# Kernel optimization log

Measured on AMD Instinct MI355X. Metric: run time of the kernel, lower is better.

The kernel has to match this reference:

```python
import jax, jax.numpy as jnp
import numpy as np

H = 512          # hidden_dim
S = 64           # num_symbols
MAXLEN = 128     # maxlen['target']
SOS = 0          # symb2int['<sos>']


def _gru_cell(x, h, Wih, Whh, bih, bhh):
    # PyTorch GRU cell. x: (N, in), h: (N, H)
    gi = x @ Wih.T + bih          # (N, 3H)
    gh = h @ Whh.T + bhh          # (N, 3H)
    ir, iz, inn = jnp.split(gi, 3, axis=-1)
    hr, hz, hn = jnp.split(gh, 3, axis=-1)
    r = jax.nn.sigmoid(ir + hr)
    z = jax.nn.sigmoid(iz + hz)
    n = jnp.tanh(inn + r * hn)
    return (1.0 - z) * n + z * h


def setup_inputs() -> dict:
    key = jax.random.key(0)
    ks = jax.random.split(key, 16)
    N, Lsrc = 128, 512
    s = 1.0 / np.sqrt(H)
    inp = {
        "x": jax.random.normal(ks[0], (N, 2, Lsrc), dtype=jnp.float32),
        "target": jax.random.randint(ks[1], (N, MAXLEN), 0, S),
        # encoder GRU (input size 2)
        "enc_Wih": jax.random.normal(ks[2], (3 * H, 2), dtype=jnp.float32) * s,
        "enc_Whh": jax.random.normal(ks[3], (3 * H, H), dtype=jnp.float32) * s,
        "enc_bih": jax.random.normal(ks[4], (3 * H,), dtype=jnp.float32) * s,
        "enc_bhh": jax.random.normal(ks[5], (3 * H,), dtype=jnp.float32) * s,
        # decoder GRU (input size H)
        "dec_Wih": jax.random.normal(ks[6], (3 * H, H), dtype=jnp.float32) * s,
        "dec_Whh": jax.random.normal(ks[7], (3 * H, H), dtype=jnp.float32) * s,
        "dec_bih": jax.random.normal(ks[8], (3 * H,), dtype=jnp.float32) * s,
        "dec_bhh": jax.random.normal(ks[9], (3 * H,), dtype=jnp.float32) * s,
        # decoder embedding, attention FF, output head
        "emb": jax.random.normal(ks[10], (S, H), dtype=jnp.float32),
        "attn_ff_W": jax.random.normal(ks[11], (H, 2 * H), dtype=jnp.float32) * s,
        "attn_ff_b": jnp.zeros((H,), dtype=jnp.float32),
        "fc_W": jax.random.normal(ks[12], (S, H), dtype=jnp.float32) * s,
        "fc_b": jnp.zeros((S,), dtype=jnp.float32),
    }
    return inp


def reference(x, target, enc_Wih, enc_Whh, enc_bih, enc_bhh,
              dec_Wih, dec_Whh, dec_bih, dec_bhh,
              emb, attn_ff_W, attn_ff_b, fc_W, fc_b):
    N = x.shape[0]
    # ---- encoder: x (N, 2, L) -> (L, N, 2), scan GRU over time ----
    xs = jnp.transpose(x, (2, 0, 1))                      # (L, N, 2)
    h0 = jnp.zeros((N, H), dtype=x.dtype)

    def enc_step(h, xt):
        h2 = _gru_cell(xt, h, enc_Wih, enc_Whh, enc_bih, enc_bhh)
        return h2, h2

    enc_hN, enc_ys = jax.lax.scan(enc_step, h0, xs)
    enc_out = jnp.transpose(enc_ys, (1, 0, 2))            # (N, L, H)

    # ---- decoder with attention, fully teacher-forced (target given) ----
    # tokens fed at step i: sos for i=0, target[:, i-1] afterwards
    toks = jnp.concatenate(
        [jnp.full((N, 1), SOS, dtype=target.dtype), target[:, :MAXLEN - 1]], axis=1)
    emb_seq = emb[toks]                                   # (N, MAXLEN, H)
    emb_seq = jnp.transpose(emb_seq, (1, 0, 2))           # (MAXLEN, N, H)

    def dec_step(h, e):
        q = _gru_cell(e, h, dec_Wih, dec_Whh, dec_bih, dec_bhh)   # (N, H)
        scores = jnp.einsum('nh,nlh->nl', q, enc_out)             # (N, L)
        w = jax.nn.softmax(scores, axis=-1)
        attn = jnp.einsum('nl,nlh->nh', w, enc_out)               # (N, H)
        ff = jnp.concatenate([q, attn], axis=-1) @ attn_ff_W.T + attn_ff_b
        dec = ff @ fc_W.T + fc_b                                  # (N, S)
        return q, (dec, w)

    dec_hN, (v_out, all_w) = jax.lax.scan(dec_step, enc_hN, emb_seq)
    v_out = jnp.transpose(v_out, (1, 0, 2))               # (N, MAXLEN, S)
    all_w = jnp.transpose(all_w, (1, 0, 2))               # (N, MAXLEN, L)
    return v_out, dec_hN[None, :, :], all_w
```

## Files before the change

### kernel.cpp

```cpp
#include <hip/hip_runtime.h>
#include <math.h>

#define H   512
#define S   64
#define T   128
#define NB  128
#define L   512

#define OFF_ENC   0u
#define OFF_Q     33554432u
#define OFF_ATTN  41943040u
#define OFF_DGI   50331648u
#define OFF_M4    50429952u
#define OFF_C     50495488u
#define OFF_FLG1  50495552u
#define OFF_FLG2  50503744u

#define OUT_V  0
#define OUT_HN 1048576
#define OUT_W  1114112

__device__ __forceinline__ float sigmoidf_(float x){ return 1.0f/(1.0f+expf(-x)); }

#define FLAG_ST(p, v) __hip_atomic_store((p), (v), __ATOMIC_RELAXED, __HIP_MEMORY_SCOPE_AGENT)
#define FLAG_LD(p)    __hip_atomic_load((p), __ATOMIC_RELAXED, __HIP_MEMORY_SCOPE_AGENT)
#define ATOM_STF(p, v) __hip_atomic_store((p), (v), __ATOMIC_RELAXED, __HIP_MEMORY_SCOPE_AGENT)
#define ATOM_LD8(p)    __hip_atomic_load((const unsigned long long*)(p), __ATOMIC_RELAXED, __HIP_MEMORY_SCOPE_AGENT)

#define GLOAD4(dst, addr) \
  asm volatile("global_load_dwordx4 %0, %1, off" : "=v"(dst) : "v"(addr))

__global__ void prep_m_kernel(float* __restrict__ M4, float* __restrict__ c,
                              const float* __restrict__ aW, const float* __restrict__ aB,
                              const float* __restrict__ fcW, const float* __restrict__ fcB){
  int idx = blockIdx.x*256 + threadIdx.x;
  int k = idx >> 6, s = idx & 63;
  float acc = 0.f;
  for (int o = 0; o < H; ++o) acc += aW[(size_t)o*1024 + k] * fcW[(size_t)s*H + o];
  int k4 = k >> 2, kk = k & 3;
  M4[(size_t)(k4*64 + s)*4 + kk] = acc;
  if (idx < 64){
    float a2 = 0.f;
    for (int o = 0; o < H; ++o) a2 += aB[o] * fcW[(size_t)idx*H + o];
    c[idx] = a2 + fcB[idx];
  }
}

__global__ __launch_bounds__(256) void dgi_kernel(
    float* __restrict__ dgi, const float* __restrict__ Wih,
    const float* __restrict__ bih, const float* __restrict__ emb){
  __shared__ __align__(16) float wsm[4][H];
  int b = blockIdx.x;
  int tid = threadIdx.x;
  int jl = tid >> 6, s = tid & 63;
  for (int jj = 0; jj < 6; ++jj){
    int j0 = b*24 + jj*4;
    __syncthreads();
    for (int e = tid; e < 512; e += 256){
      int r = e >> 7, kv = e & 127;
      ((float4*)&wsm[r][0])[kv] = *(const float4*)&Wih[(size_t)(j0+r)*H + kv*4];
    }
    __syncthreads();
    int j = j0 + jl;
    float acc = bih[j];
    #pragma unroll 4
    for (int k4 = 0; k4 < 128; ++k4){
      float4 w4 = ((const float4*)&wsm[jl][0])[k4];
      float4 e4 = *(const float4*)&emb[(size_t)s*H + k4*4];
      acc = fmaf(w4.x,e4.x, fmaf(w4.y,e4.y, fmaf(w4.z,e4.z, fmaf(w4.w,e4.w, acc))));
    }
    dgi[(size_t)s*1536 + j] = acc;
  }
}

__global__ __attribute__((amdgpu_flat_work_group_size(512,512), amdgpu_waves_per_eu(2,2)))
void enc_persist(
    float* __restrict__ enc, const float* __restrict__ x,
    const float* __restrict__ Wih, const float* __restrict__ Whh,
    const float* __restrict__ bih, const float* __restrict__ bhh,
    int* __restrict__ flags){
  __shared__ __align__(16) float hs[4*H];
  const int tid = threadIdx.x;
  const int jh_l = tid >> 3;
  const int kg   = tid & 7;
  const int g  = blockIdx.x & 31;
  const int jb = blockIdx.x >> 5;
  const int jh = jb*64 + jh_l;
  const int n0 = g*4;
  int* fl = flags + g*8*32;

  float4 wr[16], wz[16], wn[16];
  #pragma unroll
  for (int i = 0; i < 16; ++i){
    const float* p0 = &Whh[(size_t)jh*H        + (kg + 8*i)*4];
    const float* p1 = &Whh[(size_t)(512+jh)*H  + (kg + 8*i)*4];
    const float* p2 = &Whh[(size_t)(1024+jh)*H + (kg + 8*i)*4];
    GLOAD4(wr[i], p0);
    GLOAD4(wz[i], p1);
    GLOAD4(wn[i], p2);
  }
  asm volatile("s_waitcnt vmcnt(0)" ::: "memory");

  const float wir0 = Wih[jh*2],        wir1 = Wih[jh*2+1];
  const float wiz0 = Wih[(512+jh)*2],  wiz1 = Wih[(512+jh)*2+1];
  const float win0 = Wih[(1024+jh)*2], win1 = Wih[(1024+jh)*2+1];
  const float br  = bih[jh] + bhh[jh];
  const float bz  = bih[512+jh] + bhh[512+jh];
  const float bin = bih[1024+jh], bhn = bhh[1024+jh];
  const int nr = kg & 3;
  const int n = n0 + nr;
  const int sr = tid >> 7;
  const int sv = tid & 127;

  for (int t = 0; t < L; ++t){
    float x0 = x[(size_t)n*1024 + t], x1 = x[(size_t)n*1024 + 512 + t];
    if (t == 0){
      ((float4*)hs)[tid] = make_float4(0,0,0,0);
      __syncthreads();
    } else {
      if (tid < 8){
        while (FLAG_LD(&fl[tid*32]) < t) __builtin_amdgcn_s_sleep(1);
      }
      __syncthreads();
      const float* srcp = &enc[((size_t)(n0+sr)*L + (t-1))*H + sv*4];
      unsigned long long a = ATOM_LD8(srcp);
      unsigned long long b = ATOM_LD8(srcp+2);
      unsigned long long* dst = (unsigned long long*)hs;
      dst[(sr*128+sv)*2]   = a;
      dst[(sr*128+sv)*2+1] = b;
      __syncthreads();
    }

    float mar = 0.f, maz = 0.f, man = 0.f;
    #pragma unroll
    for (int nl = 0; nl < 4; ++nl){
      const float4* hb = (const float4*)&hs[nl*H];
      float pr = 0.f, pz = 0.f, pn = 0.f;
      #pragma unroll
      for (int i = 0; i < 16; ++i){
        float4 h4 = hb[kg + 8*i];
        pr = fmaf(h4.x,wr[i].x, fmaf(h4.y,wr[i].y, fmaf(h4.z,wr[i].z, fmaf(h4.w,wr[i].w, pr))));
        pz = fmaf(h4.x,wz[i].x, fmaf(h4.y,wz[i].y, fmaf(h4.z,wz[i].z, fmaf(h4.w,wz[i].w, pz))));
        pn = fmaf(h4.x,wn[i].x, fmaf(h4.y,wn[i].y, fmaf(h4.z,wn[i].z, fmaf(h4.w,wn[i].w, pn))));
      }
      #pragma unroll
      for (int off = 1; off < 8; off <<= 1){
        pr += __shfl_xor(pr, off);
        pz += __shfl_xor(pz, off);
        pn += __shfl_xor(pn, off);
      }
      if (kg == nl){ mar = pr; maz = pz; man = pn; }
    }
    if (kg < 4){
      float rg = sigmoidf_(fmaf(x0,wir0, fmaf(x1,wir1, br))  + mar);
      float zg = sigmoidf_(fmaf(x0,wiz0, fmaf(x1,wiz1, bz))  + maz);
      float ng = tanhf    (fmaf(x0,win0, fmaf(x1,win1, bin)) + rg*(man + bhn));
      float hp = hs[nr*H + jh];
      ATOM_STF(&enc[((size_t)n*L + t)*H + jh], (1.f - zg)*ng + zg*hp);
    }
    asm volatile("s_waitcnt vmcnt(0)" ::: "memory");
    __syncthreads();
    if (tid == 0) FLAG_ST(&fl[jb*32], t+1);
  }
}

__global__ __attribute__((amdgpu_flat_work_group_size(512,512), amdgpu_waves_per_eu(2,2)))
void dec_persist(
    const float* __restrict__ enc, float* __restrict__ q_all,
    const int* __restrict__ tgt, const float* __restrict__ dgi,
    const float* __restrict__ Whh, const float* __restrict__ bhh,
    float* __restrict__ hn_out, int* __restrict__ flags){
  __shared__ __align__(16) float hs[4*H];
  const int tid = threadIdx.x;
  const int jh_l = tid >> 3;
  const int kg   = tid & 7;
  const int g  = blockIdx.x & 31;
  const int jb = blockIdx.x >> 5;
  const int jh = jb*64 + jh_l;
  const int n0 = g*4;
  int* fl = flags + g*8*32;

  float4 wr[16], wz[16], wn[16];
  #pragma unroll
  for (int i = 0; i < 16; ++i){
    const float* p0 = &Whh[(size_t)jh*H        + (kg + 8*i)*4];
    const float* p1 = &Whh[(size_t)(512+jh)*H  + (kg + 8*i)*4];
    const float* p2 = &Whh[(size_t)(1024+jh)*H + (kg + 8*i)*4];
    GLOAD4(wr[i], p0);
    GLOAD4(wz[i], p1);
    GLOAD4(wn[i], p2);
  }
  asm volatile("s_waitcnt vmcnt(0)" ::: "memory");

  const float bh_r = bhh[jh], bh_z = bhh[512+jh], bh_n = bhh[1024+jh];
  const int nr = kg & 3;
  const int n = n0 + nr;
  const int sr = tid >> 7;
  const int sv = tid & 127;

  for (int t = 0; t < T; ++t){
    int tok = (t == 0) ? 0 : tgt[n*T + (t-1)];
    float g0 = dgi[(size_t)tok*1536 + jh];
    float g1 = dgi[(size_t)tok*1536 + 512 + jh];
    float g2 = dgi[(size_t)tok*1536 + 1024 + jh];
    if (t == 0){
      ((float4*)hs)[tid] = *(const float4*)&enc[((size_t)(n0+sr)*L + (L-1))*H + sv*4];
      __syncthreads();
    } else {
      if (tid < 8){
        while (FLAG_LD(&fl[tid*32]) < t) __builtin_amdgcn_s_sleep(1);
      }
      __syncthreads();
      const float* srcp = &q_all[(size_t)(t-1)*NB*H + (size_t)(n0+sr)*H + sv*4];
      unsigned long long a = ATOM_LD8(srcp);
      unsigned long long b = ATOM_LD8(srcp+2);
      unsigned long long* dst = (unsigned long long*)hs;
      dst[(sr*128+sv)*2]   = a;
      dst[(sr*128+sv)*2+1] = b;
      __syncthreads();
    }

    float mar = 0.f, maz = 0.f, man = 0.f;
    #pragma unroll
    for (int nl = 0; nl < 4; ++nl){
      const float4* hb = (const float4*)&hs[nl*H];
      float pr = 0.f, pz = 0.f, pn = 0.f;
      #pragma unroll
      for (int i = 0; i < 16; ++i){
        float4 h4 = hb[kg + 8*i];
        pr = fmaf(h4.x,wr[i].x, fmaf(h4.y,wr[i].y, fmaf(h4.z,wr[i].z, fmaf(h4.w,wr[i].w, pr))));
        pz = fmaf(h4.x,wz[i].x, fmaf(h4.y,wz[i].y, fmaf(h4.z,wz[i].z, fmaf(h4.w,wz[i].w, pz))));
        pn = fmaf(h4.x,wn[i].x, fmaf(h4.y,wn[i].y, fmaf(h4.z,wn[i].z, fmaf(h4.w,wn[i].w, pn))));
      }
      #pragma unroll
      for (int off = 1; off < 8; off <<= 1){
        pr += __shfl_xor(pr, off);
        pz += __shfl_xor(pz, off);
        pn += __shfl_xor(pn, off);
      }
      if (kg == nl){ mar = pr; maz = pz; man = pn; }
    }
    if (kg < 4){
      float rg = sigmoidf_(g0 + mar + bh_r);
      float zg = sigmoidf_(g1 + maz + bh_z);
      float ng = tanhf    (g2 + rg*(man + bh_n));
      float hp = hs[nr*H + jh];
      float q  = (1.f - zg)*ng + zg*hp;
      ATOM_STF(&q_all[(size_t)t*NB*H + (size_t)n*H + jh], q);
      if (t == T-1) hn_out[(size_t)n*H + jh] = q;
    }
    asm volatile("s_waitcnt vmcnt(0)" ::: "memory");
    __syncthreads();
    if (tid == 0) FLAG_ST(&fl[jb*32], t+1);
  }
}

__global__ __launch_bounds__(256) void scores_kernel(
    const float* __restrict__ enc, const float* __restrict__ q_all,
    float* __restrict__ wout){
  int t0 = blockIdx.x * 16, l0 = blockIdx.y * 64, n = blockIdx.z;
  int tid = threadIdx.x;
  __shared__ __align__(16) float A[16][33];
  __shared__ __align__(16) float B[32][68];
  int t_l = tid >> 4, l_g = tid & 15;
  float4 acc = make_float4(0,0,0,0);
  for (int kc = 0; kc < 16; ++kc){
    __syncthreads();
    for (int e = tid; e < 512; e += 256){
      int r = e >> 5, k = e & 31;
      A[r][k] = q_all[(size_t)(t0+r)*NB*H + (size_t)n*H + kc*32 + k];
    }
    for (int e = tid; e < 2048; e += 256){
      int l = e >> 5, k = e & 31;
      B[k][l] = enc[((size_t)n*L + l0 + l)*H + kc*32 + k];
    }
    __syncthreads();
    #pragma unroll
    for (int kk = 0; kk < 32; ++kk){
      float a = A[t_l][kk];
      float4 b = *(const float4*)&B[kk][l_g*4];
      acc.x += a*b.x; acc.y += a*b.y; acc.z += a*b.z; acc.w += a*b.w;
    }
  }
  *(float4*)&wout[(size_t)n*T*L + (size_t)(t0+t_l)*L + l0 + l_g*4] = acc;
}

__global__ __launch_bounds__(64) void softmax_kernel(float* __restrict__ w){
  float* p = w + (size_t)blockIdx.x * L;
  int lane = threadIdx.x;
  float4 v0 = *(float4*)&p[lane*8];
  float4 v1 = *(float4*)&p[lane*8+4];
  float m = fmaxf(fmaxf(fmaxf(v0.x,v0.y),fmaxf(v0.z,v0.w)),
                  fmaxf(fmaxf(v1.x,v1.y),fmaxf(v1.z,v1.w)));
  for (int off = 32; off; off >>= 1) m = fmaxf(m, __shfl_xor(m, off));
  v0.x = expf(v0.x-m); v0.y = expf(v0.y-m); v0.z = expf(v0.z-m); v0.w = expf(v0.w-m);
  v1.x = expf(v1.x-m); v1.y = expf(v1.y-m); v1.z = expf(v1.z-m); v1.w = expf(v1.w-m);
  float s = v0.x+v0.y+v0.z+v0.w+v1.x+v1.y+v1.z+v1.w;
  for (int off = 32; off; off >>= 1) s += __shfl_xor(s, off);
  float inv = 1.f/s;
  v0.x*=inv; v0.y*=inv; v0.z*=inv; v0.w*=inv;
  v1.x*=inv; v1.y*=inv; v1.z*=inv; v1.w*=inv;
  *(float4*)&p[lane*8] = v0;
  *(float4*)&p[lane*8+4] = v1;
}

__global__ __launch_bounds__(256) void attn_kernel(
    const float* __restrict__ enc, const float* __restrict__ w_in,
    float* __restrict__ attn_all){
  int t0 = blockIdx.x * 16, h0 = blockIdx.y * 64, n = blockIdx.z;
  int tid = threadIdx.x;
  __shared__ __align__(16) float A[16][33];
  __shared__ __align__(16) float B[32][64];
  int t_l = tid >> 4, h_g = tid & 15;
  float4 acc = make_float4(0,0,0,0);
  for (int lc = 0; lc < 16; ++lc){
    __syncthreads();
    for (int e = tid; e < 512; e += 256){
      int r = e >> 5, ll = e & 31;
      A[r][ll] = w_in[(size_t)n*T*L + (size_t)(t0+r)*L + lc*32 + ll];
    }
    for (int e = tid; e < 2048; e += 256){
      int ll = e >> 6, h = e & 63;
      B[ll][h] = enc[((size_t)n*L + lc*32 + ll)*H + h0 + h];
    }
    __syncthreads();
    #pragma unroll
    for (int ll = 0; ll < 32; ++ll){
      float a = A[t_l][ll];
      float4 b = *(const float4*)&B[ll][h_g*4];
      acc.x += a*b.x; acc.y += a*b.y; acc.z += a*b.z; acc.w += a*b.w;
    }
  }
  *(float4*)&attn_all[(size_t)(t0+t_l)*NB*H + (size_t)n*H + h0 + h_g*4] = acc;
}

__global__ __launch_bounds__(256) void out_kernel(
    const float* __restrict__ q_all, const float* __restrict__ attn_all,
    const float4* __restrict__ M4, const float* __restrict__ c,
    float* __restrict__ vout){
  __shared__ __align__(16) float cat[4][1024];
  int tid = threadIdx.x;
  int row0 = blockIdx.x * 4;
  for (int e = tid; e < 4096; e += 256){
    int r = e >> 10, k = e & 1023;
    int row = row0 + r;
    int n = row >> 7, t = row & 127;
    cat[r][k] = (k < 512) ? q_all[(size_t)t*NB*H + (size_t)n*H + k]
                          : attn_all[(size_t)t*NB*H + (size_t)n*H + (k-512)];
  }
  __syncthreads();
  int r_l = tid >> 6, s = tid & 63;
  int row = row0 + r_l;
  int n = row >> 7, t = row & 127;
  float acc = c[s];
  #pragma unroll 4
  for (int k4 = 0; k4 < 256; ++k4){
    float4 cv = ((const float4*)&cat[r_l][0])[k4];
    float4 m = M4[k4*64 + s];
    acc += cv.x*m.x + cv.y*m.y + cv.z*m.z + cv.w*m.w;
  }
  vout[(size_t)n*T*S + (size_t)t*S + s] = acc;
}

extern "C" void kernel_launch(void* const* d_in, const int* in_sizes, int n_in,
                              void* d_out, int out_size, void* d_ws, size_t ws_size,
                              hipStream_t stream) {
  const float* x       = (const float*)d_in[0];
  const int*   target  = (const int*)d_in[1];
  const float* enc_Wih = (const float*)d_in[2];
  const float* enc_Whh = (const float*)d_in[3];
  const float* enc_bih = (const float*)d_in[4];
  const float* enc_bhh = (const float*)d_in[5];
  const float* dec_Wih = (const float*)d_in[6];
  const float* dec_Whh = (const float*)d_in[7];
  const float* dec_bih = (const float*)d_in[8];
  const float* dec_bhh = (const float*)d_in[9];
  const float* emb     = (const float*)d_in[10];
  const float* affW    = (const float*)d_in[11];
  const float* affB    = (const float*)d_in[12];
  const float* fcW     = (const float*)d_in[13];
  const float* fcB     = (const float*)d_in[14];

  float* ws      = (float*)d_ws;
  float* enc     = ws + OFF_ENC;
  float* q_all   = ws + OFF_Q;
  float* attn_al = ws + OFF_ATTN;
  float* dgi     = ws + OFF_DGI;
  float* M4f     = ws + OFF_M4;
  float* cb      = ws + OFF_C;
  int*   flg1    = (int*)(ws + OFF_FLG1);
  int*   flg2    = (int*)(ws + OFF_FLG2);

  float* vout   = (float*)d_out + OUT_V;
  float* hn_out = (float*)d_out + OUT_HN;
  float* w_all  = (float*)d_out + OUT_W;

  hipMemsetAsync(flg1, 0, 2*8192*sizeof(int), stream);
  prep_m_kernel<<<256, 256, 0, stream>>>(M4f, cb, affW, affB, fcW, fcB);
  dgi_kernel<<<64, 256, 0, stream>>>(dgi, dec_Wih, dec_bih, emb);

  {
    void* args[] = {(void*)&enc, (void*)&x, (void*)&enc_Wih, (void*)&enc_Whh,
                    (void*)&enc_bih, (void*)&enc_bhh, (void*)&flg1};
    hipLaunchCooperativeKernel((void*)enc_persist, dim3(256), dim3(512), args, 0, stream);
  }
  {
    void* args[] = {(void*)&enc, (void*)&q_all, (void*)&target, (void*)&dgi,
                    (void*)&dec_Whh, (void*)&dec_bhh, (void*)&hn_out, (void*)&flg2};
    hipLaunchCooperativeKernel((void*)dec_persist, dim3(256), dim3(512), args, 0, stream);
  }

  scores_kernel<<<dim3(8,8,NB), 256, 0, stream>>>(enc, q_all, w_all);
  softmax_kernel<<<NB*T, 64, 0, stream>>>(w_all);
  attn_kernel<<<dim3(8,8,NB), 256, 0, stream>>>(enc, w_all, attn_al);
  out_kernel<<<NB*T/4, 256, 0, stream>>>(q_all, attn_al, (const float4*)M4f, cb, vout);
}
```

Measured before the change: 3.545 ms.

## Use per-wavefront flags and double-buffered LDS to cut barriers in persistent GRU

Replaces the per-block step flag with one flag per wavefront. Each thread now polls only the flag of the wavefront that produced the hidden-state slice it loads, instead of thread 0..7 polling and then a block barrier. Double-buffering the shared hidden state lets the end-of-step __syncthreads be removed, which drops one barrier per timestep in both the encoder and decoder recurrences. In exchange there are 8x more flags, a larger memset, and more spinning threads. Correctness relies on wave-level store/flag ordering.

```diff
diff --git a/kernel.cpp b/kernel.cpp
--- a/kernel.cpp
+++ b/kernel.cpp
@@ -14,7 +14,7 @@
 #define OFF_M4    50429952u
 #define OFF_C     50495488u
 #define OFF_FLG1  50495552u
-#define OFF_FLG2  50503744u
+#define OFF_FLG2  50561088u
 
 #define OUT_V  0
 #define OUT_HN 1048576
@@ -79,15 +79,16 @@
     const float* __restrict__ Wih, const float* __restrict__ Whh,
     const float* __restrict__ bih, const float* __restrict__ bhh,
     int* __restrict__ flags){
-  __shared__ __align__(16) float hs[4*H];
+  __shared__ __align__(16) float hs2[2][4*H];
   const int tid = threadIdx.x;
   const int jh_l = tid >> 3;
   const int kg   = tid & 7;
+  const int wv   = tid >> 6;
   const int g  = blockIdx.x & 31;
   const int jb = blockIdx.x >> 5;
   const int jh = jb*64 + jh_l;
   const int n0 = g*4;
-  int* fl = flags + g*8*32;
+  int* fl = flags + g*64*32;
 
   float4 wr[16], wz[16], wn[16];
   #pragma unroll
@@ -111,25 +112,25 @@
   const int n = n0 + nr;
   const int sr = tid >> 7;
   const int sv = tid & 127;
+  const int pf = (sv >> 1)*32;
+  const int myf = (jb*8 + wv)*32;
 
   for (int t = 0; t < L; ++t){
+    float* hs = hs2[t & 1];
     float x0 = x[(size_t)n*1024 + t], x1 = x[(size_t)n*1024 + 512 + t];
     if (t == 0){
       ((float4*)hs)[tid] = make_float4(0,0,0,0);
-      __syncthreads();
     } else {
-      if (tid < 8){
-        while (FLAG_LD(&fl[tid*32]) < t) __builtin_amdgcn_s_sleep(1);
-      }
-      __syncthreads();
+      while (FLAG_LD(&fl[pf]) < t) __builtin_amdgcn_s_sleep(1);
+      asm volatile("" ::: "memory");
       const float* srcp = &enc[((size_t)(n0+sr)*L + (t-1))*H + sv*4];
       unsigned long long a = ATOM_LD8(srcp);
       unsigned long long b = ATOM_LD8(srcp+2);
       unsigned long long* dst = (unsigned long long*)hs;
       dst[(sr*128+sv)*2]   = a;
       dst[(sr*128+sv)*2+1] = b;
-      __syncthreads();
-    }
+    }
+    __syncthreads();
 
     float mar = 0.f, maz = 0.f, man = 0.f;
     #pragma unroll
@@ -159,8 +160,7 @@
       ATOM_STF(&enc[((size_t)n*L + t)*H + jh], (1.f - zg)*ng + zg*hp);
     }
     asm volatile("s_waitcnt vmcnt(0)" ::: "memory");
-    __syncthreads();
-    if (tid == 0) FLAG_ST(&fl[jb*32], t+1);
+    if ((tid & 63) == 0) FLAG_ST(&fl[myf], t+1);
   }
 }
 
@@ -170,15 +170,16 @@
     const int* __restrict__ tgt, const float* __restrict__ dgi,
     const float* __restrict__ Whh, const float* __restrict__ bhh,
     float* __restrict__ hn_out, int* __restrict__ flags){
-  __shared__ __align__(16) float hs[4*H];
+  __shared__ __align__(16) float hs2[2][4*H];
   const int tid = threadIdx.x;
   const int jh_l = tid >> 3;
   const int kg   = tid & 7;
+  const int wv   = tid >> 6;
   const int g  = blockIdx.x & 31;
   const int jb = blockIdx.x >> 5;
   const int jh = jb*64 + jh_l;
   const int n0 = g*4;
-  int* fl = flags + g*8*32;
+  int* fl = flags + g*64*32;
 
   float4 wr[16], wz[16], wn[16];
   #pragma unroll
@@ -197,28 +198,28 @@
   const int n = n0 + nr;
   const int sr = tid >> 7;
   const int sv = tid & 127;
+  const int pf = (sv >> 1)*32;
+  const int myf = (jb*8 + wv)*32;
 
   for (int t = 0; t < T; ++t){
+    float* hs = hs2[t & 1];
     int tok = (t == 0) ? 0 : tgt[n*T + (t-1)];
     float g0 = dgi[(size_t)tok*1536 + jh];
     float g1 = dgi[(size_t)tok*1536 + 512 + jh];
     float g2 = dgi[(size_t)tok*1536 + 1024 + jh];
     if (t == 0){
       ((float4*)hs)[tid] = *(const float4*)&enc[((size_t)(n0+sr)*L + (L-1))*H + sv*4];
-      __syncthreads();
     } else {
-      if (tid < 8){
-        while (FLAG_LD(&fl[tid*32]) < t) __builtin_amdgcn_s_sleep(1);
-      }
-      __syncthreads();
+      while (FLAG_LD(&fl[pf]) < t) __builtin_amdgcn_s_sleep(1);
+      asm volatile("" ::: "memory");
       const float* srcp = &q_all[(size_t)(t-1)*NB*H + (size_t)(n0+sr)*H + sv*4];
       unsigned long long a = ATOM_LD8(srcp);
       unsigned long long b = ATOM_LD8(srcp+2);
       unsigned long long* dst = (unsigned long long*)hs;
       dst[(sr*128+sv)*2]   = a;
       dst[(sr*128+sv)*2+1] = b;
-      __syncthreads();
-    }
+    }
+    __syncthreads();
 
     float mar = 0.f, maz = 0.f, man = 0.f;
     #pragma unroll
@@ -250,8 +251,7 @@
       if (t == T-1) hn_out[(size_t)n*H + jh] = q;
     }
     asm volatile("s_waitcnt vmcnt(0)" ::: "memory");
-    __syncthreads();
-    if (tid == 0) FLAG_ST(&fl[jb*32], t+1);
+    if ((tid & 63) == 0) FLAG_ST(&fl[myf], t+1);
   }
 }
 
@@ -395,7 +395,7 @@
   float* hn_out = (float*)d_out + OUT_HN;
   float* w_all  = (float*)d_out + OUT_W;
 
-  hipMemsetAsync(flg1, 0, 2*8192*sizeof(int), stream);
+  hipMemsetAsync(flg1, 0, 2*65536*sizeof(int), stream);
   prep_m_kernel<<<256, 256, 0, stream>>>(M4f, cb, affW, affB, fcW, fcB);
   dgi_kernel<<<64, 256, 0, stream>>>(dgi, dec_Wih, dec_bih, emb);
 
```

New measurement: 4.807 ms. 1.36x slower.
